# Kernel optimization log

Measured on AMD Instinct MI355X. Metric: run time of the kernel, lower is better.

The kernel has to match this reference:

```python
import jax, jax.numpy as jnp
import numpy as np

B, L, D = 8, 8192, 512   # batch, seq_len (q_len == kv_len), model dim
H, K = 8, 64             # heads, head_dim
W = 128                  # chunk width == stride (non-overlapping chunks)


def setup_inputs() -> dict:
    key = jax.random.key(0)
    ks = jax.random.split(key, 6)
    s = 1.0 / np.sqrt(D)
    return {
        "inputs_q": jax.random.normal(ks[0], (B, L, D), jnp.float32),
        "inputs_kv": jax.random.normal(ks[1], (B, L, D), jnp.float32),
        "Wq": jax.random.normal(ks[2], (D, H, K), jnp.float32) * s,
        "Wk": jax.random.normal(ks[3], (D, H, K), jnp.float32) * s,
        "Wv": jax.random.normal(ks[4], (D, H, K), jnp.float32) * s,
        "Wo": jax.random.normal(ks[5], (H, K, D), jnp.float32) * s,
    }


def reference(inputs_q, inputs_kv, Wq, Wk, Wv, Wo):
    # LocalAttentionLayer with q/kv_chunk_width == stride == W and
    # always_attend_to_first_position=True. Since width == stride the chunks
    # are non-overlapping, so the per-chunk Python loop of the original is
    # equivalent to a batched reshape into [B, C, W, ...] chunks. QKV
    # projections are position-wise, so projecting the full sequence first is
    # exactly the same math as projecting each chunk.
    C = L // W  # number of chunks
    scale = 1.0 / jnp.sqrt(jnp.asarray(K, inputs_q.dtype))

    q = jnp.einsum('bld,dhk->blhk', inputs_q, Wq) * scale  # [B,L,H,K]
    k = jnp.einsum('bld,dhk->blhk', inputs_kv, Wk)
    v = jnp.einsum('bld,dhk->blhk', inputs_kv, Wv)

    qc = q.reshape(B, C, W, H, K)
    kc = k.reshape(B, C, W, H, K)
    vc = v.reshape(B, C, W, H, K)

    # Global first KV position ([CLS]) prepended to every chunk's keys/values,
    # matching `kv_cls = inputs_kv[..., 0:1, :]; concat([kv_cls, chunk])`.
    k_cls = jnp.broadcast_to(k[:, None, 0:1], (B, C, 1, H, K))
    v_cls = jnp.broadcast_to(v[:, None, 0:1], (B, C, 1, H, K))
    kc = jnp.concatenate([k_cls, kc], axis=2)  # [B,C,W+1,H,K]
    vc = jnp.concatenate([v_cls, vc], axis=2)

    scores = jnp.einsum('bcqhk,bcmhk->bchqm', qc, kc)  # [B,C,H,W,W+1]
    attn = jax.nn.softmax(scores, axis=-1)
    ctx = jnp.einsum('bchqm,bcmhk->bcqhk', attn, vc)   # [B,C,W,H,K]
    ctx = ctx.reshape(B, L, H, K)
    return jnp.einsum('blhk,hkd->bld', ctx, Wo)        # [B,L,D]
```

## Files before the change

kernel.cpp:

```cpp
#include <hip/hip_runtime.h>
#include <hip/hip_bf16.h>
#include <type_traits>

#define B_ 8
#define L_ 8192
#define D_ 512
#define H_ 8
#define KD_ 64
#define W_ 128
#define C_ 64
#define M_ (B_ * L_)
#define HK_ 512

typedef __bf16 bf16_t;
typedef __bf16 bf16x8 __attribute__((ext_vector_type(8)));
typedef float f32x4 __attribute__((ext_vector_type(4)));

#define GLOAD16(gp, lp)                                                        \
  __builtin_amdgcn_global_load_lds(                                            \
      (const __attribute__((address_space(1))) unsigned int*)(gp),             \
      (__attribute__((address_space(3))) unsigned int*)(lp), 16, 0, 0)

#define WAIT_LGKM0()                                                           \
  do {                                                                         \
    asm volatile("s_waitcnt lgkmcnt(0)" ::: "memory");                         \
    __builtin_amdgcn_sched_barrier(0);                                         \
  } while (0)

__global__ void prep_weights_kernel(const float* __restrict__ Wq,
                                    const float* __restrict__ Wk,
                                    const float* __restrict__ Wv,
                                    const float* __restrict__ Wo,
                                    bf16_t* __restrict__ wt) {
  const int n = blockIdx.x;
  const int mat = blockIdx.y;
  const float* src = (mat == 0) ? Wq : (mat == 1) ? Wk : (mat == 2) ? Wv : Wo;
  const float scale = (mat == 0) ? 0.125f : 1.0f;
  bf16_t* dst = wt + ((size_t)mat * 512 + n) * 512;
  for (int d = threadIdx.x; d < 512; d += blockDim.x) {
    dst[d] = (bf16_t)(src[(size_t)d * 512 + n] * scale);
  }
}

__global__ void cvt_x_kernel(const float* __restrict__ xq,
                             const float* __restrict__ xkv,
                             bf16_t* __restrict__ oq,
                             bf16_t* __restrict__ okv) {
  const float* src = blockIdx.y ? xkv : xq;
  bf16_t* dst = blockIdx.y ? okv : oq;
  const size_t e = ((size_t)blockIdx.x * blockDim.x + threadIdx.x) * 8;
  float4 a = *reinterpret_cast<const float4*>(src + e);
  float4 b = *reinterpret_cast<const float4*>(src + e + 4);
  bf16x8 o;
  o[0] = (bf16_t)a.x; o[1] = (bf16_t)a.y; o[2] = (bf16_t)a.z; o[3] = (bf16_t)a.w;
  o[4] = (bf16_t)b.x; o[5] = (bf16_t)b.y; o[6] = (bf16_t)b.z; o[7] = (bf16_t)b.w;
  *reinterpret_cast<bf16x8*>(dst + e) = o;
}

__device__ __forceinline__ bf16x8 rdfrag(const bf16_t* region, int rowbase,
                                         int lane) {
  const int fr = lane & 15;
  const int fs = (lane >> 4) ^ (lane & 3);
  return *reinterpret_cast<const bf16x8*>(region + (rowbase + fr) * 32 + fs * 8);
}

template <typename OT, int NTILE>
__global__ __launch_bounds__(512, 2)
void gemm256(const bf16_t* __restrict__ A0, const bf16_t* __restrict__ A1,
             const bf16_t* __restrict__ BT,
             OT* __restrict__ C0, OT* __restrict__ C1, OT* __restrict__ C2) {
  __shared__ bf16_t lds[8 * 8192];

  constexpr int NB = NTILE * 256;
  const int bid = blockIdx.x;
  const int swz = (bid & 7) * (NB / 8) + (bid >> 3);
  const int my = swz / NTILE;
  const int mx = swz - my * NTILE;
  const int m0 = my * 256;
  const int seg = mx >> 1;
  const int ncol0 = (mx & 1) * 256;
  const int nB0 = mx * 256;

  const bf16_t* const A = (seg == 0) ? A0 : A1;
  OT* const outp = (seg == 0) ? C0 : (seg == 1) ? C1 : C2;

  const int tid = threadIdx.x;
  const int lane = tid & 63;
  const int wid = tid >> 6;
  const int wmB = (wid >> 2) * 128;
  const int wnB = (wid & 3) * 64;

  const int sr0 = tid >> 2;
  const int sgs = (tid & 3) ^ (sr0 & 3);
  const bf16_t* const Agb = A + ((size_t)m0 + sr0) * 512 + sgs * 8;
  const bf16_t* const Bgb = BT + ((size_t)nB0 + sr0) * 512 + sgs * 8;

  auto stage = [&](int tile, int mat, int kh) {
    if (tile >= 8) return;
    bf16_t* reg = lds + (((tile & 1) * 4) + mat * 2 + kh) * 8192;
    const bf16_t* g0 = (mat == 0 ? Agb : Bgb) + tile * 64 + kh * 32;
    char* lp = (char*)reg + wid * 1024;
    GLOAD16(g0, lp);
    GLOAD16(g0 + (size_t)128 * 512, lp + 8192);
  };

  f32x4 acc[8][4] = {};
  bf16x8 a0[4], a1[4], a2[4], a3[4], b0[4], b2[4];

  stage(0, 0, 0); stage(0, 1, 0); stage(0, 0, 1); stage(0, 1, 1);
  stage(1, 1, 0); stage(1, 0, 0); stage(1, 1, 1);
  asm volatile("s_waitcnt vmcnt(6)" ::: "memory");
  __builtin_amdgcn_s_barrier();

  for (int t = 0; t < 8; ++t) {
    const int p = t & 1;
    const bf16_t* Ap0 = lds + (p * 4 + 0) * 8192;
    const bf16_t* Ap1 = lds + (p * 4 + 1) * 8192;
    const bf16_t* Bp0 = lds + (p * 4 + 2) * 8192;
    const bf16_t* Bp1 = lds + (p * 4 + 3) * 8192;

#pragma unroll
    for (int q = 0; q < 4; q++) a0[q] = rdfrag(Ap0, wmB + q * 16, lane);
#pragma unroll
    for (int q = 0; q < 4; q++) b0[q] = rdfrag(Bp0, wnB + q * 16, lane);
    stage(t + 1, 0, 1);
    __builtin_amdgcn_s_barrier();
    WAIT_LGKM0();
    if (t > 0) {
      __builtin_amdgcn_s_setprio(1);
#pragma unroll
      for (int i = 0; i < 4; i++)
#pragma unroll
        for (int j = 0; j < 4; j++)
          acc[i + 4][j] = __builtin_amdgcn_mfma_f32_16x16x32_bf16(
              a3[i], b2[j], acc[i + 4][j], 0, 0, 0);
      __builtin_amdgcn_s_setprio(0);
    }
    __builtin_amdgcn_s_barrier();

#pragma unroll
    for (int q = 0; q < 4; q++) a1[q] = rdfrag(Ap0, wmB + 64 + q * 16, lane);
    stage(t + 2, 1, 0);
    __builtin_amdgcn_s_barrier();
    WAIT_LGKM0();
    __builtin_amdgcn_s_setprio(1);
#pragma unroll
    for (int i = 0; i < 4; i++)
#pragma unroll
      for (int j = 0; j < 4; j++)
        acc[i][j] = __builtin_amdgcn_mfma_f32_16x16x32_bf16(a0[i], b0[j],
                                                            acc[i][j], 0, 0, 0);
    __builtin_amdgcn_s_setprio(0);
    __builtin_amdgcn_s_barrier();

#pragma unroll
    for (int q = 0; q < 4; q++) a2[q] = rdfrag(Ap1, wmB + q * 16, lane);
#pragma unroll
    for (int q = 0; q < 4; q++) b2[q] = rdfrag(Bp1, wnB + q * 16, lane);
    stage(t + 2, 0, 0);
    __builtin_amdgcn_s_barrier();
    WAIT_LGKM0();
    __builtin_amdgcn_s_setprio(1);
#pragma unroll
    for (int i = 0; i < 4; i++)
#pragma unroll
      for (int j = 0; j < 4; j++)
        acc[i + 4][j] = __builtin_amdgcn_mfma_f32_16x16x32_bf16(
            a1[i], b0[j], acc[i + 4][j], 0, 0, 0);
    __builtin_amdgcn_s_setprio(0);
    __builtin_amdgcn_s_barrier();

#pragma unroll
    for (int q = 0; q < 4; q++) a3[q] = rdfrag(Ap1, wmB + 64 + q * 16, lane);
    stage(t + 2, 1, 1);
    __builtin_amdgcn_s_barrier();
    WAIT_LGKM0();
    __builtin_amdgcn_s_setprio(1);
#pragma unroll
    for (int i = 0; i < 4; i++)
#pragma unroll
      for (int j = 0; j < 4; j++)
        acc[i][j] = __builtin_amdgcn_mfma_f32_16x16x32_bf16(a2[i], b2[j],
                                                            acc[i][j], 0, 0, 0);
    __builtin_amdgcn_s_setprio(0);
    if (t < 6) {
      asm volatile("s_waitcnt vmcnt(6)" ::: "memory");
    } else {
      asm volatile("s_waitcnt vmcnt(0)" ::: "memory");
    }
    __builtin_amdgcn_s_barrier();
  }

#pragma unroll
  for (int i = 0; i < 4; i++)
#pragma unroll
    for (int j = 0; j < 4; j++)
      acc[i + 4][j] = __builtin_amdgcn_mfma_f32_16x16x32_bf16(
          a3[i], b2[j], acc[i + 4][j], 0, 0, 0);

  const int crow = (lane >> 4) * 4;
  const int ccol = lane & 15;
#pragma unroll
  for (int i = 0; i < 8; i++) {
#pragma unroll
    for (int j = 0; j < 4; j++) {
      const int gm = m0 + wmB + i * 16 + crow;
      const int gn = ncol0 + wnB + j * 16 + ccol;
#pragma unroll
      for (int jj = 0; jj < 4; jj++) {
        const float vv = acc[i][j][jj];
        if constexpr (std::is_same<OT, float>::value)
          outp[(size_t)(gm + jj) * 512 + gn] = vv;
        else
          outp[(size_t)(gm + jj) * 512 + gn] = (bf16_t)vv;
      }
    }
  }
}

__global__ __launch_bounds__(256, 3)
void attn_kernel(const bf16_t* __restrict__ q, const bf16_t* __restrict__ k,
                 const bf16_t* __restrict__ v, bf16_t* __restrict__ ctx) {
  const int bid = blockIdx.x;
  const int swz = (bid & 7) * 512 + (bid >> 3);
  const int h = swz & 7;
  const int cb = swz >> 3;
  const int c = cb & 63;
  const int b = cb >> 6;

  const int tid = threadIdx.x;
  const int lane = tid & 63;
  const int w = tid >> 6;
  const int cl = lane & 15;
  const int g = lane >> 4;

  __shared__ bf16_t vT[64][136];
  __shared__ bf16_t pL[128][136];
  __shared__ float scl[128];
  __shared__ bf16_t kcls[64];
  __shared__ bf16_t vcls[64];

  const size_t headoff = (size_t)h * KD_;
  const size_t rowbase = (size_t)b * L_ + (size_t)c * W_;

  if (tid < 64) {
    kcls[tid] = k[(size_t)b * L_ * HK_ + headoff + tid];
    vcls[tid] = v[(size_t)b * L_ * HK_ + headoff + tid];
  }
  {
    const int m = tid >> 1;
    const int kd0 = (tid & 1) * 32;
    const bf16_t* vp = v + (rowbase + m) * HK_ + headoff + kd0;
#pragma unroll
    for (int i = 0; i < 4; i++) {
      bf16x8 t8 = *reinterpret_cast<const bf16x8*>(vp + i * 8);
#pragma unroll
      for (int j = 0; j < 8; j++) vT[kd0 + i * 8 + j][m] = t8[j];
    }
  }

  bf16x8 qf[2][2];
#pragma unroll
  for (int rt = 0; rt < 2; rt++)
#pragma unroll
    for (int kk = 0; kk < 2; kk++) {
      const size_t row = rowbase + w * 32 + rt * 16 + cl;
      qf[rt][kk] = *reinterpret_cast<const bf16x8*>(&q[row * HK_ + headoff + kk * 32 + g * 8]);
    }

  f32x4 sacc[2][8] = {};
#pragma unroll
  for (int ct = 0; ct < 8; ct++) {
    bf16x8 kf[2];
#pragma unroll
    for (int kk = 0; kk < 2; kk++) {
      const size_t rowm = rowbase + ct * 16 + cl;
      kf[kk] = *reinterpret_cast<const bf16x8*>(&k[rowm * HK_ + headoff + kk * 32 + g * 8]);
    }
#pragma unroll
    for (int rt = 0; rt < 2; rt++)
#pragma unroll
      for (int kk = 0; kk < 2; kk++)
        sacc[rt][ct] = __builtin_amdgcn_mfma_f32_16x16x32_bf16(qf[rt][kk], kf[kk], sacc[rt][ct], 0, 0, 0);
  }

  __syncthreads();

#pragma unroll
  for (int rt = 0; rt < 2; rt++) {
    float part = 0.f;
#pragma unroll
    for (int kk = 0; kk < 2; kk++)
#pragma unroll
      for (int j = 0; j < 8; j++)
        part += (float)qf[rt][kk][j] * (float)kcls[kk * 32 + g * 8 + j];
    part += __shfl_xor(part, 16);
    part += __shfl_xor(part, 32);
    if (g == 0) scl[w * 32 + rt * 16 + cl] = part;
  }

  float invd[2][4];
#pragma unroll
  for (int rt = 0; rt < 2; rt++) {
#pragma unroll
    for (int jj = 0; jj < 4; jj++) {
      float mx = sacc[rt][0][jj];
#pragma unroll
      for (int ct = 1; ct < 8; ct++) mx = fmaxf(mx, sacc[rt][ct][jj]);
#pragma unroll
      for (int d = 1; d < 16; d <<= 1) mx = fmaxf(mx, __shfl_xor(mx, d));
      const float sc = scl[w * 32 + rt * 16 + g * 4 + jj];
      mx = fmaxf(mx, sc);
      float sum = 0.f;
#pragma unroll
      for (int ct = 0; ct < 8; ct++) {
        const float e = __expf(sacc[rt][ct][jj] - mx);
        sacc[rt][ct][jj] = e;
        sum += e;
      }
#pragma unroll
      for (int d = 1; d < 16; d <<= 1) sum += __shfl_xor(sum, d);
      const float pc = __expf(sc - mx);
      sum += pc;
      const float inv = 1.0f / sum;
      invd[rt][jj] = inv;
      if (cl == 0) scl[w * 32 + rt * 16 + g * 4 + jj] = pc * inv;
    }
  }

#pragma unroll
  for (int rt = 0; rt < 2; rt++)
#pragma unroll
    for (int jj = 0; jj < 4; jj++) {
      const int row = w * 32 + rt * 16 + g * 4 + jj;
#pragma unroll
      for (int ct = 0; ct < 8; ct++)
        pL[row][ct * 16 + cl] = (bf16_t)(sacc[rt][ct][jj] * invd[rt][jj]);
    }
  __syncthreads();

  f32x4 cacc[2][4] = {};
#pragma unroll
  for (int kk = 0; kk < 4; kk++) {
    bf16x8 vf[4];
#pragma unroll
    for (int c2 = 0; c2 < 4; c2++)
      vf[c2] = *reinterpret_cast<const bf16x8*>(&vT[c2 * 16 + cl][kk * 32 + g * 8]);
#pragma unroll
    for (int rt = 0; rt < 2; rt++) {
      const bf16x8 pf = *reinterpret_cast<const bf16x8*>(&pL[w * 32 + rt * 16 + cl][kk * 32 + g * 8]);
#pragma unroll
      for (int c2 = 0; c2 < 4; c2++)
        cacc[rt][c2] = __builtin_amdgcn_mfma_f32_16x16x32_bf16(pf, vf[c2], cacc[rt][c2], 0, 0, 0);
    }
  }

#pragma unroll
  for (int rt = 0; rt < 2; rt++)
#pragma unroll
    for (int c2 = 0; c2 < 4; c2++)
#pragma unroll
      for (int jj = 0; jj < 4; jj++) {
        const int row = w * 32 + rt * 16 + g * 4 + jj;
        const int kd = c2 * 16 + cl;
        const float val = cacc[rt][c2][jj] + scl[row] * (float)vcls[kd];
        ctx[(rowbase + row) * HK_ + headoff + kd] = (bf16_t)val;
      }
}

extern "C" void kernel_launch(void* const* d_in, const int* in_sizes, int n_in,
                              void* d_out, int out_size, void* d_ws, size_t ws_size,
                              hipStream_t stream) {
  const float* Xq = (const float*)d_in[0];
  const float* Xkv = (const float*)d_in[1];
  const float* Wq = (const float*)d_in[2];
  const float* Wk = (const float*)d_in[3];
  const float* Wv = (const float*)d_in[4];
  const float* Wo = (const float*)d_in[5];
  float* out = (float*)d_out;

  char* ws = (char*)d_ws;
  bf16_t* wT = (bf16_t*)ws;
  size_t off = (size_t)4 * 512 * 512 * sizeof(bf16_t);
  bf16_t* xqb  = (bf16_t*)(ws + off); off += (size_t)M_ * D_ * 2;
  bf16_t* xkvb = (bf16_t*)(ws + off); off += (size_t)M_ * D_ * 2;
  bf16_t* qb = (bf16_t*)(ws + off); off += (size_t)M_ * HK_ * 2;
  bf16_t* kb = (bf16_t*)(ws + off); off += (size_t)M_ * HK_ * 2;
  bf16_t* vb = (bf16_t*)(ws + off);
  bf16_t* ctxb = xqb;

  bf16_t* wTqkv = wT;
  bf16_t* wTo = wT + (size_t)3 * 512 * 512;

  prep_weights_kernel<<<dim3(512, 4), 128, 0, stream>>>(Wq, Wk, Wv, Wo, wT);
  cvt_x_kernel<<<dim3(M_ * D_ / 8 / 256, 2), 256, 0, stream>>>(Xq, Xkv, xqb, xkvb);

  gemm256<bf16_t, 6><<<dim3(6 * (M_ / 256)), 512, 0, stream>>>(
      xqb, xkvb, wTqkv, qb, kb, vb);

  attn_kernel<<<dim3(H_ * C_ * B_), 256, 0, stream>>>(qb, kb, vb, ctxb);

  gemm256<float, 2><<<dim3(2 * (M_ / 256)), 512, 0, stream>>>(
      ctxb, ctxb, wTo, out, out, out);
}
```

Measured before the change: 366.8 us.

## Fuse fp32-to-bf16 input conversion into QKV GEMM A-tile loading

Removes the separate cvt_x kernel and has the QKV GEMM read fp32 activations directly into registers, convert to bf16 and write them to a triple-buffered LDS A region. The B operand still uses direct global-to-LDS loads with double buffering. This avoids writing and re-reading bf16 copies of both inputs. In exchange the A path now goes through registers with higher register and LDS pressure, and each of the 6 N-tile blocks re-reads fp32 A at twice the bytes. The LDS swizzle pattern also changes in both GEMMs.

```diff
diff --git a/kernel.cpp b/kernel.cpp
--- a/kernel.cpp
+++ b/kernel.cpp
@@ -42,34 +42,61 @@
   }
 }
 
-__global__ void cvt_x_kernel(const float* __restrict__ xq,
-                             const float* __restrict__ xkv,
-                             bf16_t* __restrict__ oq,
-                             bf16_t* __restrict__ okv) {
-  const float* src = blockIdx.y ? xkv : xq;
-  bf16_t* dst = blockIdx.y ? okv : oq;
-  const size_t e = ((size_t)blockIdx.x * blockDim.x + threadIdx.x) * 8;
-  float4 a = *reinterpret_cast<const float4*>(src + e);
-  float4 b = *reinterpret_cast<const float4*>(src + e + 4);
-  bf16x8 o;
-  o[0] = (bf16_t)a.x; o[1] = (bf16_t)a.y; o[2] = (bf16_t)a.z; o[3] = (bf16_t)a.w;
-  o[4] = (bf16_t)b.x; o[5] = (bf16_t)b.y; o[6] = (bf16_t)b.z; o[7] = (bf16_t)b.w;
-  *reinterpret_cast<bf16x8*>(dst + e) = o;
-}
-
 __device__ __forceinline__ bf16x8 rdfrag(const bf16_t* region, int rowbase,
                                          int lane) {
   const int fr = lane & 15;
-  const int fs = (lane >> 4) ^ (lane & 3);
+  const int fs = (lane >> 4) ^ ((lane >> 2) & 2);
   return *reinterpret_cast<const bf16x8*>(region + (rowbase + fr) * 32 + fs * 8);
 }
 
-template <typename OT, int NTILE>
+__device__ __forceinline__ void aload_f32(const float* Af, int m0, int tid,
+                                          int tt, float4 (&ar)[4][2]) {
+  const int r = tid >> 1, kh = tid & 1;
+  const float* base = Af + (size_t)(m0 + r) * 512 + tt * 64 + kh * 32;
+#pragma unroll
+  for (int s = 0; s < 4; s++) {
+    const int p = (s + ((r >> 1) & 3)) & 3;
+    const int cg = p ^ (((r >> 3) & 1) << 1);
+    ar[s][0] = *reinterpret_cast<const float4*>(base + cg * 8);
+    ar[s][1] = *reinterpret_cast<const float4*>(base + cg * 8 + 4);
+  }
+}
+
+__device__ __forceinline__ void awrite_f32(bf16_t* Abufs, int tid, int tt,
+                                           const float4 (&ar)[4][2]) {
+  const int r = tid >> 1, kh = tid & 1;
+  bf16_t* reg = Abufs + ((tt % 3) * 2 + kh) * 8192;
+#pragma unroll
+  for (int s = 0; s < 4; s++) {
+    const int p = (s + ((r >> 1) & 3)) & 3;
+    bf16x8 o;
+    o[0] = (bf16_t)ar[s][0].x; o[1] = (bf16_t)ar[s][0].y;
+    o[2] = (bf16_t)ar[s][0].z; o[3] = (bf16_t)ar[s][0].w;
+    o[4] = (bf16_t)ar[s][1].x; o[5] = (bf16_t)ar[s][1].y;
+    o[6] = (bf16_t)ar[s][1].z; o[7] = (bf16_t)ar[s][1].w;
+    *reinterpret_cast<bf16x8*>(&reg[r * 32 + p * 8]) = o;
+  }
+}
+
+#define MFMA16(AF, BF, ACC, OFF)                                               \
+  do {                                                                         \
+    __builtin_amdgcn_s_setprio(1);                                             \
+    _Pragma("unroll") for (int i_ = 0; i_ < 4; i_++)                           \
+        _Pragma("unroll") for (int j_ = 0; j_ < 4; j_++)                       \
+            ACC[i_ + OFF][j_] = __builtin_amdgcn_mfma_f32_16x16x32_bf16(       \
+                AF[i_], BF[j_], ACC[i_ + OFF][j_], 0, 0, 0);                   \
+    __builtin_amdgcn_s_setprio(0);                                             \
+  } while (0)
+
+template <int NTILE>
 __global__ __launch_bounds__(512, 2)
-void gemm256(const bf16_t* __restrict__ A0, const bf16_t* __restrict__ A1,
-             const bf16_t* __restrict__ BT,
-             OT* __restrict__ C0, OT* __restrict__ C1, OT* __restrict__ C2) {
-  __shared__ bf16_t lds[8 * 8192];
+void gemm_qkv(const float* __restrict__ A0f, const float* __restrict__ A1f,
+              const bf16_t* __restrict__ BT,
+              bf16_t* __restrict__ C0, bf16_t* __restrict__ C1,
+              bf16_t* __restrict__ C2) {
+  __shared__ __align__(16) bf16_t lds[81920];
+  bf16_t* const Abufs = lds;
+  bf16_t* const Bbufs = lds + 49152;
 
   constexpr int NB = NTILE * 256;
   const int bid = blockIdx.x;
@@ -81,8 +108,8 @@
   const int ncol0 = (mx & 1) * 256;
   const int nB0 = mx * 256;
 
-  const bf16_t* const A = (seg == 0) ? A0 : A1;
-  OT* const outp = (seg == 0) ? C0 : (seg == 1) ? C1 : C2;
+  const float* const Af = (seg == 0) ? A0f : A1f;
+  bf16_t* const outp = (seg == 0) ? C0 : (seg == 1) ? C1 : C2;
 
   const int tid = threadIdx.x;
   const int lane = tid & 63;
@@ -91,13 +118,129 @@
   const int wnB = (wid & 3) * 64;
 
   const int sr0 = tid >> 2;
-  const int sgs = (tid & 3) ^ (sr0 & 3);
-  const bf16_t* const Agb = A + ((size_t)m0 + sr0) * 512 + sgs * 8;
+  const int sgs = (tid & 3) ^ (((sr0 >> 3) & 1) << 1);
+  const bf16_t* const Bgb = BT + ((size_t)nB0 + sr0) * 512 + sgs * 8;
+
+  auto bstage = [&](int tile, int kh) {
+    if (tile >= 8) return;
+    bf16_t* reg = Bbufs + ((tile & 1) * 2 + kh) * 8192;
+    const bf16_t* g0 = Bgb + tile * 64 + kh * 32;
+    char* lp = (char*)reg + wid * 1024;
+    GLOAD16(g0, lp);
+    GLOAD16(g0 + (size_t)128 * 512, lp + 8192);
+  };
+
+  f32x4 acc[8][4] = {};
+  bf16x8 a0[4], a1[4], a2[4], a3[4], b0[4], b2[4];
+  float4 ar[4][2];
+
+  {
+    float4 ar0[4][2], ar1[4][2];
+    aload_f32(Af, m0, tid, 0, ar0);
+    aload_f32(Af, m0, tid, 1, ar1);
+    bstage(0, 0); bstage(0, 1); bstage(1, 0); bstage(1, 1);
+    awrite_f32(Abufs, tid, 0, ar0);
+    awrite_f32(Abufs, tid, 1, ar1);
+    asm volatile("s_waitcnt vmcnt(0) lgkmcnt(0)" ::: "memory");
+    __builtin_amdgcn_s_barrier();
+  }
+
+  for (int t = 0; t < 8; ++t) {
+    const int pA = t % 3;
+    const int pB = t & 1;
+    const bf16_t* AR0 = Abufs + (pA * 2 + 0) * 8192;
+    const bf16_t* AR1 = Abufs + (pA * 2 + 1) * 8192;
+    const bf16_t* BR0 = Bbufs + (pB * 2 + 0) * 8192;
+    const bf16_t* BR1 = Bbufs + (pB * 2 + 1) * 8192;
+
+#pragma unroll
+    for (int q = 0; q < 4; q++) a0[q] = rdfrag(AR0, wmB + q * 16, lane);
+#pragma unroll
+    for (int q = 0; q < 4; q++) b0[q] = rdfrag(BR0, wnB + q * 16, lane);
+    if (t < 6) aload_f32(Af, m0, tid, t + 2, ar);
+    __builtin_amdgcn_s_barrier();
+    WAIT_LGKM0();
+    if (t > 0) MFMA16(a3, b2, acc, 4);
+    __builtin_amdgcn_s_barrier();
+
+#pragma unroll
+    for (int q = 0; q < 4; q++) a1[q] = rdfrag(AR0, wmB + 64 + q * 16, lane);
+    if (t < 6) bstage(t + 2, 0);
+    __builtin_amdgcn_s_barrier();
+    WAIT_LGKM0();
+    MFMA16(a0, b0, acc, 0);
+    __builtin_amdgcn_s_barrier();
+
+#pragma unroll
+    for (int q = 0; q < 4; q++) a2[q] = rdfrag(AR1, wmB + q * 16, lane);
+#pragma unroll
+    for (int q = 0; q < 4; q++) b2[q] = rdfrag(BR1, wnB + q * 16, lane);
+    __builtin_amdgcn_s_barrier();
+    WAIT_LGKM0();
+    MFMA16(a1, b0, acc, 4);
+    __builtin_amdgcn_s_barrier();
+
+#pragma unroll
+    for (int q = 0; q < 4; q++) a3[q] = rdfrag(AR1, wmB + 64 + q * 16, lane);
+    if (t < 6) awrite_f32(Abufs, tid, t + 2, ar);
+    if (t < 6) bstage(t + 2, 1);
+    __builtin_amdgcn_s_barrier();
+    WAIT_LGKM0();
+    MFMA16(a2, b2, acc, 0);
+    if (t < 6) {
+      asm volatile("s_waitcnt vmcnt(4)" ::: "memory");
+    } else {
+      asm volatile("s_waitcnt vmcnt(0)" ::: "memory");
+    }
+    __builtin_amdgcn_s_barrier();
+  }
+
+  MFMA16(a3, b2, acc, 4);
+
+  const int crow = (lane >> 4) * 4;
+  const int ccol = lane & 15;
+#pragma unroll
+  for (int i = 0; i < 8; i++) {
+#pragma unroll
+    for (int j = 0; j < 4; j++) {
+      const int gm = m0 + wmB + i * 16 + crow;
+      const int gn = ncol0 + wnB + j * 16 + ccol;
+#pragma unroll
+      for (int jj = 0; jj < 4; jj++)
+        outp[(size_t)(gm + jj) * 512 + gn] = (bf16_t)acc[i][j][jj];
+    }
+  }
+}
+
+template <typename OT, int NTILE>
+__global__ __launch_bounds__(512, 2)
+void gemm256(const bf16_t* __restrict__ A0, const bf16_t* __restrict__ BT,
+             OT* __restrict__ C0) {
+  __shared__ __align__(16) bf16_t lds[65536];
+
+  constexpr int NB = NTILE * 256;
+  const int bid = blockIdx.x;
+  const int swz = (bid & 7) * (NB / 8) + (bid >> 3);
+  const int my = swz / NTILE;
+  const int mx = swz - my * NTILE;
+  const int m0 = my * 256;
+  const int ncol0 = (mx & 1) * 256;
+  const int nB0 = mx * 256;
+
+  const int tid = threadIdx.x;
+  const int lane = tid & 63;
+  const int wid = tid >> 6;
+  const int wmB = (wid >> 2) * 128;
+  const int wnB = (wid & 3) * 64;
+
+  const int sr0 = tid >> 2;
+  const int sgs = (tid & 3) ^ (((sr0 >> 3) & 1) << 1);
+  const bf16_t* const Agb = A0 + ((size_t)m0 + sr0) * 512 + sgs * 8;
   const bf16_t* const Bgb = BT + ((size_t)nB0 + sr0) * 512 + sgs * 8;
 
   auto stage = [&](int tile, int mat, int kh) {
     if (tile >= 8) return;
-    bf16_t* reg = lds + (((tile & 1) * 4) + mat * 2 + kh) * 8192;
+    bf16_t* reg = lds + ((tile & 1) * 4 + mat * 2 + kh) * 8192;
     const bf16_t* g0 = (mat == 0 ? Agb : Bgb) + tile * 64 + kh * 32;
     char* lp = (char*)reg + wid * 1024;
     GLOAD16(g0, lp);
@@ -126,16 +269,7 @@
     stage(t + 1, 0, 1);
     __builtin_amdgcn_s_barrier();
     WAIT_LGKM0();
-    if (t > 0) {
-      __builtin_amdgcn_s_setprio(1);
-#pragma unroll
-      for (int i = 0; i < 4; i++)
-#pragma unroll
-        for (int j = 0; j < 4; j++)
-          acc[i + 4][j] = __builtin_amdgcn_mfma_f32_16x16x32_bf16(
-              a3[i], b2[j], acc[i + 4][j], 0, 0, 0);
-      __builtin_amdgcn_s_setprio(0);
-    }
+    if (t > 0) MFMA16(a3, b2, acc, 4);
     __builtin_amdgcn_s_barrier();
 
 #pragma unroll
@@ -143,14 +277,7 @@
     stage(t + 2, 1, 0);
     __builtin_amdgcn_s_barrier();
     WAIT_LGKM0();
-    __builtin_amdgcn_s_setprio(1);
-#pragma unroll
-    for (int i = 0; i < 4; i++)
-#pragma unroll
-      for (int j = 0; j < 4; j++)
-        acc[i][j] = __builtin_amdgcn_mfma_f32_16x16x32_bf16(a0[i], b0[j],
-                                                            acc[i][j], 0, 0, 0);
-    __builtin_amdgcn_s_setprio(0);
+    MFMA16(a0, b0, acc, 0);
     __builtin_amdgcn_s_barrier();
 
 #pragma unroll
@@ -160,14 +287,7 @@
     stage(t + 2, 0, 0);
     __builtin_amdgcn_s_barrier();
     WAIT_LGKM0();
-    __builtin_amdgcn_s_setprio(1);
-#pragma unroll
-    for (int i = 0; i < 4; i++)
-#pragma unroll
-      for (int j = 0; j < 4; j++)
-        acc[i + 4][j] = __builtin_amdgcn_mfma_f32_16x16x32_bf16(
-            a1[i], b0[j], acc[i + 4][j], 0, 0, 0);
-    __builtin_amdgcn_s_setprio(0);
+    MFMA16(a1, b0, acc, 4);
     __builtin_amdgcn_s_barrier();
 
 #pragma unroll
@@ -175,14 +295,7 @@
     stage(t + 2, 1, 1);
     __builtin_amdgcn_s_barrier();
     WAIT_LGKM0();
-    __builtin_amdgcn_s_setprio(1);
-#pragma unroll
-    for (int i = 0; i < 4; i++)
-#pragma unroll
-      for (int j = 0; j < 4; j++)
-        acc[i][j] = __builtin_amdgcn_mfma_f32_16x16x32_bf16(a2[i], b2[j],
-                                                            acc[i][j], 0, 0, 0);
-    __builtin_amdgcn_s_setprio(0);
+    MFMA16(a2, b2, acc, 0);
     if (t < 6) {
       asm volatile("s_waitcnt vmcnt(6)" ::: "memory");
     } else {
@@ -191,12 +304,7 @@
     __builtin_amdgcn_s_barrier();
   }
 
-#pragma unroll
-  for (int i = 0; i < 4; i++)
-#pragma unroll
-    for (int j = 0; j < 4; j++)
-      acc[i + 4][j] = __builtin_amdgcn_mfma_f32_16x16x32_bf16(
-          a3[i], b2[j], acc[i + 4][j], 0, 0, 0);
+  MFMA16(a3, b2, acc, 4);
 
   const int crow = (lane >> 4) * 4;
   const int ccol = lane & 15;
@@ -210,9 +318,9 @@
       for (int jj = 0; jj < 4; jj++) {
         const float vv = acc[i][j][jj];
         if constexpr (std::is_same<OT, float>::value)
-          outp[(size_t)(gm + jj) * 512 + gn] = vv;
+          C0[(size_t)(gm + jj) * 512 + gn] = vv;
         else
-          outp[(size_t)(gm + jj) * 512 + gn] = (bf16_t)vv;
+          C0[(size_t)(gm + jj) * 512 + gn] = (bf16_t)vv;
       }
     }
   }
@@ -382,24 +490,20 @@
   char* ws = (char*)d_ws;
   bf16_t* wT = (bf16_t*)ws;
   size_t off = (size_t)4 * 512 * 512 * sizeof(bf16_t);
-  bf16_t* xqb  = (bf16_t*)(ws + off); off += (size_t)M_ * D_ * 2;
-  bf16_t* xkvb = (bf16_t*)(ws + off); off += (size_t)M_ * D_ * 2;
   bf16_t* qb = (bf16_t*)(ws + off); off += (size_t)M_ * HK_ * 2;
   bf16_t* kb = (bf16_t*)(ws + off); off += (size_t)M_ * HK_ * 2;
-  bf16_t* vb = (bf16_t*)(ws + off);
-  bf16_t* ctxb = xqb;
+  bf16_t* vb = (bf16_t*)(ws + off); off += (size_t)M_ * HK_ * 2;
+  bf16_t* ctxb = (bf16_t*)(ws + off);
 
   bf16_t* wTqkv = wT;
   bf16_t* wTo = wT + (size_t)3 * 512 * 512;
 
   prep_weights_kernel<<<dim3(512, 4), 128, 0, stream>>>(Wq, Wk, Wv, Wo, wT);
-  cvt_x_kernel<<<dim3(M_ * D_ / 8 / 256, 2), 256, 0, stream>>>(Xq, Xkv, xqb, xkvb);
-
-  gemm256<bf16_t, 6><<<dim3(6 * (M_ / 256)), 512, 0, stream>>>(
-      xqb, xkvb, wTqkv, qb, kb, vb);
+
+  gemm_qkv<6><<<dim3(6 * (M_ / 256)), 512, 0, stream>>>(
+      Xq, Xkv, wTqkv, qb, kb, vb);
 
   attn_kernel<<<dim3(H_ * C_ * B_), 256, 0, stream>>>(qb, kb, vb, ctxb);
 
-  gemm256<float, 2><<<dim3(2 * (M_ / 256)), 512, 0, stream>>>(
-      ctxb, ctxb, wTo, out, out, out);
-}
+  gemm256<float, 2><<<dim3(2 * (M_ / 256)), 512, 0, stream>>>(ctxb, wTo, out);
+}
```

Result: slower. 446.0 us (+21.6%).
